# Kernel optimization log

Measured on AMD Instinct MI355X. Metric: run time of the kernel, lower is better.

The kernel has to match this reference:

```python
import jax, jax.numpy as jnp
import numpy as np

HIDDEN = 768
HEADS = 12
HEAD_DIM = HIDDEN // HEADS
ORDER = 5


def setup_inputs() -> dict:
    key = jax.random.key(0)
    ks = jax.random.split(key, 8)
    s = 0.02
    return {
        "hidden_states": jax.random.normal(ks[0], (4, 2048, HIDDEN), jnp.float32),
        "Wq": jax.random.normal(ks[1], (HIDDEN, HIDDEN), jnp.float32) * s,
        "bq": jnp.zeros((HIDDEN,), jnp.float32),
        "Wk": jax.random.normal(ks[2], (HIDDEN, HIDDEN), jnp.float32) * s,
        "bk": jnp.zeros((HIDDEN,), jnp.float32),
        "Wv": jax.random.normal(ks[3], (HIDDEN, HIDDEN), jnp.float32) * s,
        "bv": jnp.zeros((HIDDEN,), jnp.float32),
        "alphas": jax.random.normal(ks[4], (HEADS, ORDER + 1), jnp.float32) * s,
    }


def _chebyshev_bias(alphas, seq_len, dtype):
    pos = jnp.arange(seq_len, dtype=dtype)
    # rel[i, j] = j - i, normalized to [-1, 1]
    denom = dtype.type(max(seq_len - 1, 1)) if hasattr(dtype, 'type') else float(max(seq_len - 1, 1))
    x = jnp.clip((pos[None, :] - pos[:, None]) / float(max(seq_len - 1, 1)), -1.0, 1.0)
    t0 = jnp.ones_like(x)
    polys = [t0, x]
    for _ in range(2, ORDER + 1):
        polys.append(2.0 * x * polys[-1] - polys[-2])
    tk = jnp.stack(polys, axis=-1)  # [S, S, order+1]
    return jnp.einsum('hk,ijk->hij', alphas, tk)  # [H, S, S]


def reference(hidden_states, Wq, bq, Wk, bk, Wv, bv, alphas):
    b, s, _ = hidden_states.shape

    def split_heads(t):
        return t.reshape(b, s, HEADS, HEAD_DIM).transpose(0, 2, 1, 3)

    q = split_heads(hidden_states @ Wq.T + bq)  # [B, H, S, D]
    k = split_heads(hidden_states @ Wk.T + bk)
    v = split_heads(hidden_states @ Wv.T + bv)

    scores = jnp.einsum('bhid,bhjd->bhij', q, k) / jnp.sqrt(
        jnp.asarray(HEAD_DIM, hidden_states.dtype))
    scores = scores + _chebyshev_bias(alphas, s, hidden_states.dtype)[None]
    probs = jax.nn.softmax(scores, axis=-1)
    ctx = jnp.einsum('bhij,bhjd->bhid', probs, v)  # [B, H, S, D]
    return ctx.transpose(0, 2, 1, 3).reshape(b, s, HIDDEN)
```

## Files before the change

### kernel.cpp

```cpp
#include <hip/hip_runtime.h>
#include <hip/hip_fp16.h>

#define HIDDEN 768
#define HEADS 12
#define HDIM 64
#define SEQ 2048
#define BATCH 4
#define ORDER 5
#define LOG2E 1.44269504088896f

typedef _Float16 f16;
typedef _Float16 f16x8 __attribute__((ext_vector_type(8)));
typedef _Float16 f16x4 __attribute__((ext_vector_type(4)));
typedef float f32x4 __attribute__((ext_vector_type(4)));

#define MFMA16x16x32(A, B, C) __builtin_amdgcn_mfma_f32_16x16x32_f16(A, B, C, 0, 0, 0)

#define GLD16(gptr, lptr)                                                     \
    __builtin_amdgcn_global_load_lds(                                         \
        (const __attribute__((address_space(1))) void*)(gptr),                \
        (__attribute__((address_space(3))) void*)(lptr), 16, 0, 0)

#define NXG (8192 * 768 / 8)
#define NWG (768 * 768 / 8)
#define NCVT (NXG + 3 * NWG)
#define NBIAS (HEADS * (2 * SEQ - 1))

__global__ __launch_bounds__(256)
void prep_kernel(const float* __restrict__ X,
                 const float* __restrict__ Wq, const float* __restrict__ Wk,
                 const float* __restrict__ Wv, const float* __restrict__ alphas,
                 f16* __restrict__ Xh, f16* __restrict__ Wh,
                 float* __restrict__ biasTab)
{
    const int tid = blockIdx.x * 256 + threadIdx.x;
    if (tid < NCVT) {
        const float* src;
        f16* dst;
        size_t off;
        if (tid < NXG)               { src = X;  dst = Xh;              off = (size_t)tid * 8; }
        else if (tid < NXG + NWG)    { src = Wq; dst = Wh;              off = (size_t)(tid - NXG) * 8; }
        else if (tid < NXG + 2*NWG)  { src = Wk; dst = Wh + 768 * 768;  off = (size_t)(tid - NXG - NWG) * 8; }
        else                         { src = Wv; dst = Wh + 2*768*768;  off = (size_t)(tid - NXG - 2*NWG) * 8; }
        float4 a = *(const float4*)(src + off);
        float4 b = *(const float4*)(src + off + 4);
        f16x8 h;
        h[0] = (f16)a.x; h[1] = (f16)a.y; h[2] = (f16)a.z; h[3] = (f16)a.w;
        h[4] = (f16)b.x; h[5] = (f16)b.y; h[6] = (f16)b.z; h[7] = (f16)b.w;
        *(f16x8*)(dst + off) = h;
    } else {
        int idx = tid - NCVT;
        if (idx >= NBIAS) return;
        const int W = 2 * SEQ - 1;
        int h = idx / W;
        int t = idx - h * W;
        float x = (float)(t - (SEQ - 1)) / (float)(SEQ - 1);
        float tp = 1.0f;
        float tc = x;
        float acc = alphas[h * (ORDER + 1) + 0] * tp + alphas[h * (ORDER + 1) + 1] * tc;
#pragma unroll
        for (int k = 2; k <= ORDER; ++k) {
            float tn = 2.0f * x * tc - tp;
            acc += alphas[h * (ORDER + 1) + k] * tn;
            tp = tc; tc = tn;
        }
        biasTab[idx] = acc * LOG2E;
    }
}

__global__ __launch_bounds__(256)
void qkv_kernel(const f16* __restrict__ Xh, const f16* __restrict__ Wh,
                const float* __restrict__ bq, const float* __restrict__ bk,
                const float* __restrict__ bv,
                f16* __restrict__ qf, f16* __restrict__ kf, f16* __restrict__ vtf)
{
    const int wgid = (blockIdx.x & 7) * 144 + (blockIdx.x >> 3);
    const int tileM = wgid / 18;
    const int tileN = wgid % 18;
    const int m0 = tileM * 128;
    const int n0g = tileN * 128;
    const int w = tileN / 6;
    const int nloc0 = n0g - w * 768;
    const float* __restrict__ bias = (w == 0) ? bq : (w == 1) ? bk : bv;

    __shared__ __align__(16) f16 sA[128][32];
    __shared__ __align__(16) f16 sB[128][32];

    const int t = threadIdx.x;
    const int lane = t & 63;
    const int wv = t >> 6;
    const int wm = wv >> 1, wn = wv & 1;
    const int fr = lane & 15;
    const int kg = lane >> 4;

    const int srow = lane >> 2;
    const int scol = (lane & 3) * 8;

    f32x4 acc[4][4];
#pragma unroll
    for (int i = 0; i < 4; ++i)
#pragma unroll
        for (int j = 0; j < 4; ++j) acc[i][j] = (f32x4)(0.0f);

    const f16* gA = Xh + (size_t)(m0 + wv * 32 + srow) * 768 + scol;
    const f16* gB = Wh + (size_t)(n0g + wv * 32 + srow) * 768 + scol;
    f16* lA0 = &sA[wv * 32][0];
    f16* lA1 = &sA[wv * 32 + 16][0];
    f16* lB0 = &sB[wv * 32][0];
    f16* lB1 = &sB[wv * 32 + 16][0];

    for (int kt = 0; kt < 768; kt += 32) {
        __syncthreads();
        GLD16(gA + kt, lA0);
        GLD16(gA + kt + 16 * 768, lA1);
        GLD16(gB + kt, lB0);
        GLD16(gB + kt + 16 * 768, lB1);
        __syncthreads();

        f16x8 af[4], bf[4];
#pragma unroll
        for (int i = 0; i < 4; ++i) {
            af[i] = *(const f16x8*)&sA[wm * 64 + i * 16 + fr][kg * 8];
            bf[i] = *(const f16x8*)&sB[wn * 64 + i * 16 + fr][kg * 8];
        }
#pragma unroll
        for (int mi = 0; mi < 4; ++mi)
#pragma unroll
            for (int ni = 0; ni < 4; ++ni)
                acc[mi][ni] = MFMA16x16x32(af[mi], bf[ni], acc[mi][ni]);
    }

    const int bb = m0 >> 11;
#pragma unroll
    for (int mi = 0; mi < 4; ++mi) {
        const int s0 = (m0 & 2047) + wm * 64 + mi * 16 + kg * 4;
#pragma unroll
        for (int ni = 0; ni < 4; ++ni) {
            const int nloc = nloc0 + wn * 64 + ni * 16 + fr;
            const int hh = nloc >> 6, d = nloc & 63;
            const size_t bh = (size_t)bb * HEADS + hh;
            const float bc = bias[nloc];
            if (w == 2) {
                f16x4 pv;
#pragma unroll
                for (int r = 0; r < 4; ++r) pv[r] = (f16)(acc[mi][ni][r] + bc);
                *(f16x4*)&vtf[(bh * HDIM + d) * SEQ + s0] = pv;
            } else if (w == 0) {
#pragma unroll
                for (int r = 0; r < 4; ++r)
                    qf[(bh * SEQ + s0 + r) * HDIM + d] =
                        (f16)((acc[mi][ni][r] + bc) * (0.125f * LOG2E));
            } else {
#pragma unroll
                for (int r = 0; r < 4; ++r)
                    kf[(bh * SEQ + s0 + r) * HDIM + d] = (f16)(acc[mi][ni][r] + bc);
            }
        }
    }
}

#define LDK 72

struct __align__(16) SMem {
    union {
        struct {
            f16 sK[64][LDK];
            f16 sVT[64][LDK];
        } kv;
        float sO[4][16][LDK];
    } u;
    f16 sP[4][32][LDK];
    float sBias[2176];
};

__global__ __launch_bounds__(256, 3)
void attn_kernel(const f16* __restrict__ qf, const f16* __restrict__ kf,
                 const f16* __restrict__ vtf, const float* __restrict__ biasTab,
                 float* __restrict__ out)
{
    const int qt = blockIdx.x & 15;
    const int bh = blockIdx.x >> 4;
    const int h = bh % HEADS;
    const int b = bh / HEADS;
    const int q0 = qt * 128;

    __shared__ SMem sm;

    const int t = threadIdx.x;
    const int lane = t & 63;
    const int wv = t >> 6;
    const int fr = lane & 15;
    const int kg = lane >> 4;

    {
        const float* bsrc = biasTab + (size_t)h * (2 * SEQ - 1) + 1920 - q0;
        for (int u = t; u < 2175; u += 256) sm.sBias[u] = bsrc[u];
    }

    f16x8 aq[2][2];
#pragma unroll
    for (int s = 0; s < 2; ++s)
#pragma unroll
        for (int c = 0; c < 2; ++c)
            aq[s][c] = *(const f16x8*)(qf +
                ((size_t)bh * SEQ + q0 + wv * 32 + s * 16 + fr) * HDIM + c * 32 + kg * 8);

    f32x4 oacc[2][4];
    float lsum[2] = {0.0f, 0.0f};
#pragma unroll
    for (int s = 0; s < 2; ++s)
#pragma unroll
        for (int df = 0; df < 4; ++df) oacc[s][df] = (f32x4)(0.0f);

    for (int j0 = 0; j0 < SEQ; j0 += 64) {
        __syncthreads();
        {
            int row = t >> 2, cc = (t & 3) * 16;
            const f16* ks = kf + ((size_t)bh * SEQ + j0 + row) * HDIM + cc;
            *(f16x8*)&sm.u.kv.sK[row][cc]     = *(const f16x8*)(ks);
            *(f16x8*)&sm.u.kv.sK[row][cc + 8] = *(const f16x8*)(ks + 8);
            const f16* vs = vtf + ((size_t)bh * HDIM + row) * SEQ + j0 + cc;
            *(f16x8*)&sm.u.kv.sVT[row][cc]     = *(const f16x8*)(vs);
            *(f16x8*)&sm.u.kv.sVT[row][cc + 8] = *(const f16x8*)(vs + 8);
        }
        __syncthreads();

        f32x4 tt[2][4];
#pragma unroll
        for (int s = 0; s < 2; ++s)
#pragma unroll
            for (int ni = 0; ni < 4; ++ni) tt[s][ni] = (f32x4)(0.0f);
#pragma unroll
        for (int ni = 0; ni < 4; ++ni) {
            f16x8 bk0 = *(const f16x8*)&sm.u.kv.sK[ni * 16 + fr][kg * 8];
            f16x8 bk1 = *(const f16x8*)&sm.u.kv.sK[ni * 16 + fr][32 + kg * 8];
            tt[0][ni] = MFMA16x16x32(bk0, aq[0][0], tt[0][ni]);
            tt[0][ni] = MFMA16x16x32(bk1, aq[0][1], tt[0][ni]);
            tt[1][ni] = MFMA16x16x32(bk0, aq[1][0], tt[1][ni]);
            tt[1][ni] = MFMA16x16x32(bk1, aq[1][1], tt[1][ni]);
        }

        const int ub = j0 + kg * 4 - wv * 32 - fr + 127;
        float bb[5][4];
#pragma unroll
        for (int g = 0; g < 5; ++g)
#pragma unroll
            for (int r = 0; r < 4; ++r)
                bb[g][r] = sm.sBias[ub + (g - 1) * 16 + r];

#pragma unroll
        for (int s = 0; s < 2; ++s) {
            float ls = 0.0f;
#pragma unroll
            for (int ni = 0; ni < 4; ++ni) {
                f16x4 ph;
#pragma unroll
                for (int r = 0; r < 4; ++r) {
                    float p = __builtin_amdgcn_exp2f(tt[s][ni][r] + bb[ni - s + 1][r]);
                    ls += p;
                    ph[r] = (f16)p;
                }
                *(f16x4*)&sm.sP[wv][s * 16 + fr][ni * 16 + kg * 4] = ph;
            }
            lsum[s] += ls;
        }

        f16x8 ap00 = *(const f16x8*)&sm.sP[wv][fr][kg * 8];
        f16x8 ap01 = *(const f16x8*)&sm.sP[wv][fr][32 + kg * 8];
        f16x8 ap10 = *(const f16x8*)&sm.sP[wv][16 + fr][kg * 8];
        f16x8 ap11 = *(const f16x8*)&sm.sP[wv][16 + fr][32 + kg * 8];
#pragma unroll
        for (int df = 0; df < 4; ++df) {
            f16x8 bv0 = *(const f16x8*)&sm.u.kv.sVT[df * 16 + fr][kg * 8];
            f16x8 bv1 = *(const f16x8*)&sm.u.kv.sVT[df * 16 + fr][32 + kg * 8];
            oacc[0][df] = MFMA16x16x32(bv0, ap00, oacc[0][df]);
            oacc[0][df] = MFMA16x16x32(bv1, ap01, oacc[0][df]);
            oacc[1][df] = MFMA16x16x32(bv0, ap10, oacc[1][df]);
            oacc[1][df] = MFMA16x16x32(bv1, ap11, oacc[1][df]);
        }
    }

    float inv[2];
#pragma unroll
    for (int s = 0; s < 2; ++s) {
        float l = lsum[s];
        l += __shfl_xor(l, 16, 64);
        l += __shfl_xor(l, 32, 64);
        inv[s] = 1.0f / l;
    }

    __syncthreads();
#pragma unroll
    for (int s = 0; s < 2; ++s) {
#pragma unroll
        for (int df = 0; df < 4; ++df) {
            f32x4 v = oacc[s][df];
            v *= inv[s];
            *(f32x4*)&sm.u.sO[wv][fr][df * 16 + kg * 4] = v;
        }
        int row = lane >> 2;
        int cb = (lane & 3) * 16;
        float* dst = out + ((size_t)b * SEQ + q0 + wv * 32 + s * 16 + row) * HIDDEN
                         + h * HDIM + cb;
#pragma unroll
        for (int i = 0; i < 4; ++i) {
            f32x4 v = *(const f32x4*)&sm.u.sO[wv][row][cb + 4 * i];
            *(f32x4*)(dst + 4 * i) = v;
        }
    }
}

extern "C" void kernel_launch(void* const* d_in, const int* in_sizes, int n_in,
                              void* d_out, int out_size, void* d_ws, size_t ws_size,
                              hipStream_t stream) {
    const float* X      = (const float*)d_in[0];
    const float* Wq     = (const float*)d_in[1];
    const float* bq     = (const float*)d_in[2];
    const float* Wk     = (const float*)d_in[3];
    const float* bk     = (const float*)d_in[4];
    const float* Wv     = (const float*)d_in[5];
    const float* bv     = (const float*)d_in[6];
    const float* alphas = (const float*)d_in[7];
    float* out = (float*)d_out;

    const size_t nQ = (size_t)BATCH * HEADS * SEQ * HDIM;
    f16* qf  = (f16*)d_ws;
    f16* kf  = qf + nQ;
    f16* vtf = kf + nQ;
    float* biasTab = (float*)(vtf + nQ);
    f16* Xh = (f16*)(biasTab + 49152);
    f16* Wh = Xh + (size_t)8192 * 768;

    const int prep_threads = NCVT + NBIAS;
    hipLaunchKernelGGL(prep_kernel, dim3((prep_threads + 255) / 256), dim3(256), 0,
                       stream, X, Wq, Wk, Wv, alphas, Xh, Wh, biasTab);
    hipLaunchKernelGGL(qkv_kernel, dim3(1152), dim3(256), 0, stream,
                       Xh, Wh, bq, bk, bv, qf, kf, vtf);
    hipLaunchKernelGGL(attn_kernel, dim3(BATCH * HEADS * 16), dim3(256), 0, stream,
                       qf, kf, vtf, biasTab, out);
}
```

Measured before the change: 141.3 us.

## Double-buffer K/V tiles with async global_load_lds, XOR swizzle and XCD-aware mapping

The attention kernel now stages K and V^T tiles straight into LDS with global_load_lds into two buffers, prefetching the next tile while the current one is computed. This removes one barrier per iteration and the register round-trip for staging. LDS padding is replaced by an XOR swizzle on K, V and P tiles to avoid bank conflicts without the extra space. The bias table is stored in fp16 to shrink LDS use, and blocks are remapped so the query tiles of one head land on the same XCD for better L2 reuse. The cost is slightly lower bias precision and an extra barrier in the epilogue.

```diff
diff --git a/kernel.cpp b/kernel.cpp
--- a/kernel.cpp
+++ b/kernel.cpp
@@ -159,18 +159,13 @@
     }
 }
 
-#define LDK 72
-
 struct __align__(16) SMem {
     union {
-        struct {
-            f16 sK[64][LDK];
-            f16 sVT[64][LDK];
-        } kv;
-        float sO[4][16][LDK];
+        f16 kv[2][2][64][64];
+        float sO[4][16][72];
     } u;
-    f16 sP[4][32][LDK];
-    float sBias[2176];
+    f16 sP[4][32][64];
+    f16 sBiasH[2304];
 };
 
 __global__ __launch_bounds__(256, 3)
@@ -178,8 +173,10 @@
                  const f16* __restrict__ vtf, const float* __restrict__ biasTab,
                  float* __restrict__ out)
 {
-    const int qt = blockIdx.x & 15;
-    const int bh = blockIdx.x >> 4;
+    const int xcd = blockIdx.x & 7;
+    const int ii = blockIdx.x >> 3;
+    const int qt = ii & 15;
+    const int bh = (ii >> 4) * 8 + xcd;
     const int h = bh % HEADS;
     const int b = bh / HEADS;
     const int q0 = qt * 128;
@@ -191,10 +188,11 @@
     const int wv = t >> 6;
     const int fr = lane & 15;
     const int kg = lane >> 4;
+    const int r7 = fr & 7;
 
     {
         const float* bsrc = biasTab + (size_t)h * (2 * SEQ - 1) + 1920 - q0;
-        for (int u = t; u < 2175; u += 256) sm.sBias[u] = bsrc[u];
+        for (int u = t; u < 2175; u += 256) sm.sBiasH[u] = (f16)bsrc[u];
     }
 
     f16x8 aq[2][2];
@@ -205,6 +203,17 @@
             aq[s][c] = *(const f16x8*)(qf +
                 ((size_t)bh * SEQ + q0 + wv * 32 + s * 16 + fr) * HDIM + c * 32 + kg * 8);
 
+    auto stage = [&](int buf, int j0) {
+        const int lrow = lane >> 3;
+        const int sw = 8 * ((lane & 7) ^ lrow);
+        const f16* gk = kf + ((size_t)bh * SEQ + j0 + wv * 16 + lrow) * HDIM + sw;
+        GLD16(gk,            &sm.u.kv[buf][0][wv * 16][0]);
+        GLD16(gk + 8 * HDIM, &sm.u.kv[buf][0][wv * 16 + 8][0]);
+        const f16* gv = vtf + ((size_t)bh * HDIM + wv * 16 + lrow) * SEQ + j0 + sw;
+        GLD16(gv,           &sm.u.kv[buf][1][wv * 16][0]);
+        GLD16(gv + 8 * SEQ, &sm.u.kv[buf][1][wv * 16 + 8][0]);
+    };
+
     f32x4 oacc[2][4];
     float lsum[2] = {0.0f, 0.0f};
 #pragma unroll
@@ -212,18 +221,12 @@
 #pragma unroll
         for (int df = 0; df < 4; ++df) oacc[s][df] = (f32x4)(0.0f);
 
+    int cur = 0;
+    stage(0, 0);
+
     for (int j0 = 0; j0 < SEQ; j0 += 64) {
         __syncthreads();
-        {
-            int row = t >> 2, cc = (t & 3) * 16;
-            const f16* ks = kf + ((size_t)bh * SEQ + j0 + row) * HDIM + cc;
-            *(f16x8*)&sm.u.kv.sK[row][cc]     = *(const f16x8*)(ks);
-            *(f16x8*)&sm.u.kv.sK[row][cc + 8] = *(const f16x8*)(ks + 8);
-            const f16* vs = vtf + ((size_t)bh * HDIM + row) * SEQ + j0 + cc;
-            *(f16x8*)&sm.u.kv.sVT[row][cc]     = *(const f16x8*)(vs);
-            *(f16x8*)&sm.u.kv.sVT[row][cc + 8] = *(const f16x8*)(vs + 8);
-        }
-        __syncthreads();
+        if (j0 + 64 < SEQ) stage(cur ^ 1, j0 + 64);
 
         f32x4 tt[2][4];
 #pragma unroll
@@ -232,8 +235,9 @@
             for (int ni = 0; ni < 4; ++ni) tt[s][ni] = (f32x4)(0.0f);
 #pragma unroll
         for (int ni = 0; ni < 4; ++ni) {
-            f16x8 bk0 = *(const f16x8*)&sm.u.kv.sK[ni * 16 + fr][kg * 8];
-            f16x8 bk1 = *(const f16x8*)&sm.u.kv.sK[ni * 16 + fr][32 + kg * 8];
+            const f16* kb = &sm.u.kv[cur][0][ni * 16 + fr][0];
+            f16x8 bk0 = *(const f16x8*)(kb + 8 * (kg ^ r7));
+            f16x8 bk1 = *(const f16x8*)(kb + 8 * ((kg + 4) ^ r7));
             tt[0][ni] = MFMA16x16x32(bk0, aq[0][0], tt[0][ni]);
             tt[0][ni] = MFMA16x16x32(bk1, aq[0][1], tt[0][ni]);
             tt[1][ni] = MFMA16x16x32(bk0, aq[1][0], tt[1][ni]);
@@ -246,7 +250,7 @@
         for (int g = 0; g < 5; ++g)
 #pragma unroll
             for (int r = 0; r < 4; ++r)
-                bb[g][r] = sm.sBias[ub + (g - 1) * 16 + r];
+                bb[g][r] = (float)sm.sBiasH[ub + (g - 1) * 16 + r];
 
 #pragma unroll
         for (int s = 0; s < 2; ++s) {
@@ -260,24 +264,29 @@
                     ls += p;
                     ph[r] = (f16)p;
                 }
-                *(f16x4*)&sm.sP[wv][s * 16 + fr][ni * 16 + kg * 4] = ph;
+                *(f16x4*)&sm.sP[wv][s * 16 + fr]
+                    [(((ni * 2 + (kg >> 1)) ^ r7) * 8) + (kg & 1) * 4] = ph;
             }
             lsum[s] += ls;
         }
 
-        f16x8 ap00 = *(const f16x8*)&sm.sP[wv][fr][kg * 8];
-        f16x8 ap01 = *(const f16x8*)&sm.sP[wv][fr][32 + kg * 8];
-        f16x8 ap10 = *(const f16x8*)&sm.sP[wv][16 + fr][kg * 8];
-        f16x8 ap11 = *(const f16x8*)&sm.sP[wv][16 + fr][32 + kg * 8];
+        const f16* pb0 = &sm.sP[wv][fr][0];
+        const f16* pb1 = &sm.sP[wv][16 + fr][0];
+        f16x8 ap00 = *(const f16x8*)(pb0 + 8 * (kg ^ r7));
+        f16x8 ap01 = *(const f16x8*)(pb0 + 8 * ((kg + 4) ^ r7));
+        f16x8 ap10 = *(const f16x8*)(pb1 + 8 * (kg ^ r7));
+        f16x8 ap11 = *(const f16x8*)(pb1 + 8 * ((kg + 4) ^ r7));
 #pragma unroll
         for (int df = 0; df < 4; ++df) {
-            f16x8 bv0 = *(const f16x8*)&sm.u.kv.sVT[df * 16 + fr][kg * 8];
-            f16x8 bv1 = *(const f16x8*)&sm.u.kv.sVT[df * 16 + fr][32 + kg * 8];
+            const f16* vb = &sm.u.kv[cur][1][df * 16 + fr][0];
+            f16x8 bv0 = *(const f16x8*)(vb + 8 * (kg ^ r7));
+            f16x8 bv1 = *(const f16x8*)(vb + 8 * ((kg + 4) ^ r7));
             oacc[0][df] = MFMA16x16x32(bv0, ap00, oacc[0][df]);
             oacc[0][df] = MFMA16x16x32(bv1, ap01, oacc[0][df]);
             oacc[1][df] = MFMA16x16x32(bv0, ap10, oacc[1][df]);
             oacc[1][df] = MFMA16x16x32(bv1, ap11, oacc[1][df]);
         }
+        cur ^= 1;
     }
 
     float inv[2];
@@ -307,6 +316,7 @@
             f32x4 v = *(const f32x4*)&sm.u.sO[wv][row][cb + 4 * i];
             *(f32x4*)(dst + 4 * i) = v;
         }
+        __syncthreads();
     }
 }
 
```

After: 161.5 us. 1.14x slower.

## Prefetch next K/V tile into registers, fold bias into MFMA init, remap blocks per XCD

Applied to the files above, without the earlier changes.

The K and V^T global loads for the next 64-key tile are now issued into registers at the start of each iteration and written to LDS after the current tile's compute, so load latency overlaps the MFMA and exp work. The bias is preloaded into the QK^T accumulators, which removes the per-element add before exp2. s_setprio raises wave priority around the MFMA blocks, and the block index is remapped so that blocks sharing a batch-head land on the same XCD for better L2 reuse of K and V. The cost is higher register pressure from the staged registers, which could lower occupancy under launch_bounds(256,3).

```diff
diff --git a/kernel.cpp b/kernel.cpp
--- a/kernel.cpp
+++ b/kernel.cpp
@@ -178,8 +178,10 @@
                  const f16* __restrict__ vtf, const float* __restrict__ biasTab,
                  float* __restrict__ out)
 {
-    const int qt = blockIdx.x & 15;
-    const int bh = blockIdx.x >> 4;
+    const int xcd = blockIdx.x & 7;
+    const int ii = blockIdx.x >> 3;
+    const int qt = ii & 15;
+    const int bh = (ii >> 4) * 8 + xcd;
     const int h = bh % HEADS;
     const int b = bh / HEADS;
     const int q0 = qt * 128;
@@ -212,24 +214,50 @@
 #pragma unroll
         for (int df = 0; df < 4; ++df) oacc[s][df] = (f32x4)(0.0f);
 
+    const int srow = t >> 2;
+    const int scol = (t & 3) * 16;
+    const f16* const gkb = kf + ((size_t)bh * SEQ + srow) * HDIM + scol;
+    const f16* const gvb = vtf + ((size_t)bh * HDIM + srow) * SEQ + scol;
+
+    f16x8 rk0, rk1, rv0, rv1;
+    auto stage_load = [&](int j0) {
+        rk0 = *(const f16x8*)(gkb + (size_t)j0 * HDIM);
+        rk1 = *(const f16x8*)(gkb + (size_t)j0 * HDIM + 8);
+        rv0 = *(const f16x8*)(gvb + j0);
+        rv1 = *(const f16x8*)(gvb + j0 + 8);
+    };
+    auto stage_write = [&]() {
+        *(f16x8*)&sm.u.kv.sK[srow][scol]      = rk0;
+        *(f16x8*)&sm.u.kv.sK[srow][scol + 8]  = rk1;
+        *(f16x8*)&sm.u.kv.sVT[srow][scol]     = rv0;
+        *(f16x8*)&sm.u.kv.sVT[srow][scol + 8] = rv1;
+    };
+
+    stage_load(0);
+    stage_write();
+    __syncthreads();
+
     for (int j0 = 0; j0 < SEQ; j0 += 64) {
-        __syncthreads();
-        {
-            int row = t >> 2, cc = (t & 3) * 16;
-            const f16* ks = kf + ((size_t)bh * SEQ + j0 + row) * HDIM + cc;
-            *(f16x8*)&sm.u.kv.sK[row][cc]     = *(const f16x8*)(ks);
-            *(f16x8*)&sm.u.kv.sK[row][cc + 8] = *(const f16x8*)(ks + 8);
-            const f16* vs = vtf + ((size_t)bh * HDIM + row) * SEQ + j0 + cc;
-            *(f16x8*)&sm.u.kv.sVT[row][cc]     = *(const f16x8*)(vs);
-            *(f16x8*)&sm.u.kv.sVT[row][cc + 8] = *(const f16x8*)(vs + 8);
-        }
-        __syncthreads();
+        const bool more = (j0 + 64 < SEQ);
+        if (more) stage_load(j0 + 64);
+
+        const int ub = j0 + kg * 4 - wv * 32 - fr + 127;
+        float bbv[5][4];
+#pragma unroll
+        for (int g = 0; g < 5; ++g)
+#pragma unroll
+            for (int r = 0; r < 4; ++r)
+                bbv[g][r] = sm.sBias[ub + (g - 1) * 16 + r];
 
         f32x4 tt[2][4];
 #pragma unroll
         for (int s = 0; s < 2; ++s)
 #pragma unroll
-            for (int ni = 0; ni < 4; ++ni) tt[s][ni] = (f32x4)(0.0f);
+            for (int ni = 0; ni < 4; ++ni)
+#pragma unroll
+                for (int r = 0; r < 4; ++r) tt[s][ni][r] = bbv[ni - s + 1][r];
+
+        __builtin_amdgcn_s_setprio(1);
 #pragma unroll
         for (int ni = 0; ni < 4; ++ni) {
             f16x8 bk0 = *(const f16x8*)&sm.u.kv.sK[ni * 16 + fr][kg * 8];
@@ -239,14 +267,7 @@
             tt[1][ni] = MFMA16x16x32(bk0, aq[1][0], tt[1][ni]);
             tt[1][ni] = MFMA16x16x32(bk1, aq[1][1], tt[1][ni]);
         }
-
-        const int ub = j0 + kg * 4 - wv * 32 - fr + 127;
-        float bb[5][4];
-#pragma unroll
-        for (int g = 0; g < 5; ++g)
-#pragma unroll
-            for (int r = 0; r < 4; ++r)
-                bb[g][r] = sm.sBias[ub + (g - 1) * 16 + r];
+        __builtin_amdgcn_s_setprio(0);
 
 #pragma unroll
         for (int s = 0; s < 2; ++s) {
@@ -256,7 +277,7 @@
                 f16x4 ph;
 #pragma unroll
                 for (int r = 0; r < 4; ++r) {
-                    float p = __builtin_amdgcn_exp2f(tt[s][ni][r] + bb[ni - s + 1][r]);
+                    float p = __builtin_amdgcn_exp2f(tt[s][ni][r]);
                     ls += p;
                     ph[r] = (f16)p;
                 }
@@ -269,6 +290,7 @@
         f16x8 ap01 = *(const f16x8*)&sm.sP[wv][fr][32 + kg * 8];
         f16x8 ap10 = *(const f16x8*)&sm.sP[wv][16 + fr][kg * 8];
         f16x8 ap11 = *(const f16x8*)&sm.sP[wv][16 + fr][32 + kg * 8];
+        __builtin_amdgcn_s_setprio(1);
 #pragma unroll
         for (int df = 0; df < 4; ++df) {
             f16x8 bv0 = *(const f16x8*)&sm.u.kv.sVT[df * 16 + fr][kg * 8];
@@ -277,6 +299,13 @@
             oacc[0][df] = MFMA16x16x32(bv1, ap01, oacc[0][df]);
             oacc[1][df] = MFMA16x16x32(bv0, ap10, oacc[1][df]);
             oacc[1][df] = MFMA16x16x32(bv1, ap11, oacc[1][df]);
+        }
+        __builtin_amdgcn_s_setprio(0);
+
+        __syncthreads();
+        if (more) {
+            stage_write();
+            __syncthreads();
         }
     }
 
```

Measured after the change: 136.0 us. -3.7%, faster.
